# Kernel tuning notes

Measured on AMD Instinct MI355X. Metric: run time of the kernel, lower is better.

## Reference

```python
import jax, jax.numpy as jnp
import numpy as np

DIM = 384
WIN = 7
HEADS = 12
N = WIN * WIN
B_ = 4096
NW = 64


def _relative_position_index(ws: int) -> np.ndarray:
    coords = np.stack(np.meshgrid(np.arange(ws), np.arange(ws), indexing='ij'))  # (2, ws, ws)
    flat = coords.reshape(2, -1)  # (2, N)
    rel = flat[:, :, None] - flat[:, None, :]  # (2, N, N)
    rel = rel.transpose(1, 2, 0).copy()  # (N, N, 2)
    rel[:, :, 0] += ws - 1
    rel[:, :, 1] += ws - 1
    rel[:, :, 0] *= 2 * ws - 1
    return rel.sum(-1).astype(np.int32)  # (N, N)


def setup_inputs() -> dict:
    key = jax.random.key(0)
    ks = jax.random.split(key, 6)
    x = jax.random.normal(ks[0], (B_, N, DIM), dtype=jnp.float32)
    mask = jnp.zeros((NW, N, N), dtype=jnp.float32)
    bias_table = 0.02 * jax.random.normal(ks[1], ((2 * WIN - 1) ** 2, HEADS), dtype=jnp.float32)
    qkv_w = jax.random.normal(ks[2], (3 * DIM, DIM), dtype=jnp.float32) / np.sqrt(DIM)
    qkv_b = jnp.zeros((3 * DIM,), dtype=jnp.float32)
    proj_w = jax.random.normal(ks[3], (DIM, DIM), dtype=jnp.float32) / np.sqrt(DIM)
    proj_b = jnp.zeros((DIM,), dtype=jnp.float32)
    rel_index = jnp.asarray(_relative_position_index(WIN))  # (N, N) int32
    return {"x": x, "mask": mask, "bias_table": bias_table, "qkv_w": qkv_w,
            "qkv_b": qkv_b, "proj_w": proj_w, "proj_b": proj_b, "rel_index": rel_index}


def reference(x, mask, bias_table, qkv_w, qkv_b, proj_w, proj_b, rel_index):
    Bw, n, c = x.shape
    h = bias_table.shape[1]
    d = c // h
    scale = d ** (-0.5)
    # qkv projection: (Bw, n, 3, h, d)
    qkv = (x @ qkv_w.T + qkv_b).reshape(Bw, n, 3, h, d)
    qkv = jnp.transpose(qkv, (2, 0, 3, 1, 4))  # (3, Bw, h, n, d)
    q, k, v = qkv[0], qkv[1], qkv[2]
    attn = jnp.einsum('bhqd,bhkd->bhqk', q * scale, k)  # (Bw, h, n, n)
    bias = bias_table[rel_index]  # (n, n, h)
    attn = attn + jnp.transpose(bias, (2, 0, 1))[None]  # broadcast over Bw
    nW = mask.shape[0]
    attn = attn.reshape(Bw // nW, nW, h, n, n) + mask[None, :, None]
    attn = attn.reshape(Bw, h, n, n)
    attn = jax.nn.softmax(attn, axis=-1)
    out = jnp.einsum('bhqk,bhkd->bhqd', attn, v)  # (Bw, h, n, d)
    out = jnp.transpose(out, (0, 2, 1, 3)).reshape(Bw, n, c)
    return out @ proj_w.T + proj_b
```

## Files before the change

kernel.cpp:

```cpp
#include <hip/hip_runtime.h>
#include <hip/hip_bf16.h>

#define DIM   384
#define NWIN  49
#define HEADS 12
#define SCALE 0.17677669529663687f

typedef unsigned short ushort;
using bf16x8 = __attribute__((ext_vector_type(8))) short;
using u16x4  = __attribute__((ext_vector_type(4))) ushort;
using f32x4  = __attribute__((ext_vector_type(4))) float;

__device__ __forceinline__ ushort f2bf(float f) {
  unsigned u = __float_as_uint(f);
  u += 0x7fff + ((u >> 16) & 1);
  return (ushort)(u >> 16);
}

typedef __attribute__((address_space(1))) const void gas_void;
typedef __attribute__((address_space(3))) void las_void;

__device__ __forceinline__ void gload16(const ushort* g, ushort* l) {
  __builtin_amdgcn_global_load_lds((gas_void*)g, (las_void*)l, 16, 0, 0);
}

__global__ void prep_kernel(const float* __restrict__ qkv_w, const float* __restrict__ proj_w,
                            const float* __restrict__ bias_table, const int* __restrict__ rel_index,
                            const float* __restrict__ mask, const float* __restrict__ qkv_b,
                            ushort* __restrict__ wqb, ushort* __restrict__ wpb,
                            float* __restrict__ qbF, float* __restrict__ bmL) {
  int i0 = blockIdx.x * 256 + threadIdx.x;
  int stride = gridDim.x * 256;
  for (int i = i0; i < 1152 * 384; i += stride) {
    float v = qkv_w[i];
    if (i < 384 * 384) v *= SCALE;
    wqb[i] = f2bf(v);
  }
  for (int i = i0; i < 384 * 384; i += stride) wpb[i] = f2bf(proj_w[i]);
  for (int i = i0; i < 1152; i += stride) qbF[i] = qkv_b[i] * (i < 384 ? SCALE : 1.f);
  for (int i = i0; i < 64 * HEADS * 4 * 4 * 4 * 64; i += stride) {
    int l = i & 63, r = (i >> 6) & 3, kt = (i >> 8) & 3, wq = (i >> 10) & 3;
    int hw = i >> 12;
    int h = hw % 12, wdx = hw / 12;
    int q = wq * 16 + (l >> 4) * 4 + r;
    int key = kt * 16 + (l & 15);
    float v;
    if (q < NWIN)
      v = (key < NWIN) ? bias_table[rel_index[q * NWIN + key] * HEADS + h]
                         + mask[wdx * (NWIN * NWIN) + q * NWIN + key]
                       : -3.0e38f;
    else
      v = 0.f;
    bmL[i] = v;
  }
}

#define WB_OFF 0
#define QS_OFF 24576
#define KS_OFF 29696
#define VT_OFF 34816
#define AO_OFF 39424
#define SMEM_US 77056

__global__ __launch_bounds__(512, 2) void winattn_kernel(
    const float* __restrict__ x, const float* __restrict__ qbF,
    const float* __restrict__ proj_b, const ushort* __restrict__ wqb,
    const ushort* __restrict__ wpb, const float* __restrict__ bmL,
    float* __restrict__ out)
{
  extern __shared__ ushort smem[];
  ushort* wb = smem + WB_OFF;
  ushort* ao = smem + AO_OFF;

  const int blk = blockIdx.x;
  const int tid = threadIdx.x;
  const int w = tid >> 6, l = tid & 63;
  const int c = l & 15, g = l >> 4;
  const int wm = w >> 1, wn = w & 1;
  const int win = w >> 2, wq = w & 3;
  const float LOG2E = 1.4426950408889634f;

  ushort* qsw = smem + QS_OFF + win * 2560;
  ushort* ksw = smem + KS_OFF + win * 2560;
  ushort* vtw = smem + VT_OFF + win * 2304;
  ushort* psw = qsw;

  auto stage_qkv = [&](int h, int kc, int buf) {
    #pragma unroll
    for (int s = 0; s < 3; ++s) {
      int i = s * 512 + tid;
      int n = i >> 4, g16 = i & 15;
      int grow = (n >> 5) * 384 + h * 32 + (n & 31);
      int sg = (g16 & 8) | ((g16 & 7) ^ (n & 7));
      gload16(wqb + (size_t)grow * DIM + kc * 128 + (sg << 3),
              wb + buf * 12288 + i * 8);
    }
  };
  auto stage_proj = [&](int nb, int kc, int buf) {
    #pragma unroll
    for (int s = 0; s < 3; ++s) {
      int i = s * 512 + tid;
      int n = i >> 4, g16 = i & 15;
      int grow = nb * 96 + n;
      int sg = (g16 & 8) | ((g16 & 7) ^ (n & 7));
      gload16(wpb + (size_t)grow * DIM + kc * 128 + (sg << 3),
              wb + buf * 12288 + i * 8);
    }
  };

  bf16x8 areg[2][12] = {};
  auto compute_qkv = [&](int kcC, int buf, f32x4 (&acc)[2][3]) {
    const ushort* wcb = wb + buf * 12288;
    #pragma unroll
    for (int kk = 0; kk < 4; ++kk) {
      int sB = ((kk * 4 + g) ^ (c & 7)) << 3;
      #pragma unroll
      for (int nt = 0; nt < 3; ++nt) {
        int n = (wn * 3 + nt) * 16 + c;
        bf16x8 bb = *(const bf16x8*)&wcb[n * 128 + sB];
        acc[0][nt] = __builtin_amdgcn_mfma_f32_16x16x32_bf16(areg[0][kcC * 4 + kk], bb, acc[0][nt], 0, 0, 0);
        acc[1][nt] = __builtin_amdgcn_mfma_f32_16x16x32_bf16(areg[1][kcC * 4 + kk], bb, acc[1][nt], 0, 0, 0);
      }
    }
  };
  auto compute_proj = [&](int kcC, int buf, f32x4 (&acc)[2][3]) {
    const ushort* wcb = wb + buf * 12288;
    int r0 = wm * 32 + c;      if (r0 >= 98) r0 -= 64;
    int r1 = wm * 32 + 16 + c; if (r1 >= 98) r1 -= 64;
    #pragma unroll
    for (int kk = 0; kk < 4; ++kk) {
      int p = kcC * 16 + kk * 4 + g;
      int sw = (p ^ (c & 7)) << 3;
      bf16x8 a0 = *(const bf16x8*)&ao[r0 * 384 + sw];
      bf16x8 a1 = *(const bf16x8*)&ao[r1 * 384 + sw];
      int sB = ((kk * 4 + g) ^ (c & 7)) << 3;
      #pragma unroll
      for (int nt = 0; nt < 3; ++nt) {
        int n = (wn * 3 + nt) * 16 + c;
        bf16x8 bb = *(const bf16x8*)&wcb[n * 128 + sB];
        acc[0][nt] = __builtin_amdgcn_mfma_f32_16x16x32_bf16(a0, bb, acc[0][nt], 0, 0, 0);
        acc[1][nt] = __builtin_amdgcn_mfma_f32_16x16x32_bf16(a1, bb, acc[1][nt], 0, 0, 0);
      }
    }
  };

  stage_qkv(0, 0, 0);
  stage_qkv(0, 1, 1);
  {
    const float* xb = x + (size_t)blk * (2 * NWIN * DIM);
    for (int i = tid; i < 9408; i += 512) {
      float4 f = ((const float4*)xb)[i];
      int row = i / 96;
      int c4 = i - row * 96;
      int k = c4 * 4;
      int gr = k >> 3;
      u16x4 v4 = { f2bf(f.x), f2bf(f.y), f2bf(f.z), f2bf(f.w) };
      *(u16x4*)&ao[row * 384 + ((gr ^ (row & 7)) << 3) + (k & 7)] = v4;
    }
  }
  __syncthreads();

  #pragma unroll
  for (int mt = 0; mt < 2; ++mt) {
    int row = wm * 32 + mt * 16 + c;
    int wi = row >> 6, tok = row & 63;
    if (tok < NWIN) {
      int ar = wi * 49 + tok;
      #pragma unroll
      for (int kg = 0; kg < 12; ++kg) {
        int gx = kg * 4 + g;
        areg[mt][kg] = *(const bf16x8*)&ao[ar * 384 + ((gx ^ (ar & 7)) << 3)];
      }
    }
  }

  for (int h = 0; h < HEADS; ++h) {
    f32x4 acc[2][3] = {};
    const int par = h & 1;

    compute_qkv(0, par, acc);
    __syncthreads();
    stage_qkv(h, 2, par);

    compute_qkv(1, par ^ 1, acc);
    __syncthreads();
    if (h < 11) stage_qkv(h + 1, 0, par ^ 1); else stage_proj(0, 0, par ^ 1);

    compute_qkv(2, par, acc);
    __syncthreads();
    if (h < 11) stage_qkv(h + 1, 1, par); else stage_proj(0, 1, par);

    {
      int winE = wm >> 1;
      ushort* qsE = smem + QS_OFF + winE * 2560;
      ushort* ksE = smem + KS_OFF + winE * 2560;
      ushort* vtE = smem + VT_OFF + winE * 2304;
      #pragma unroll
      for (int nt = 0; nt < 3; ++nt) {
        int gnt = wn * 3 + nt;
        int which = gnt >> 1;
        int d = (gnt & 1) * 16 + c;
        float qb_ = qbF[which * 384 + h * 32 + d];
        #pragma unroll
        for (int mt = 0; mt < 2; ++mt) {
          #pragma unroll
          for (int r = 0; r < 4; ++r) {
            int tok = (wm & 1) * 32 + mt * 16 + g * 4 + r;
            float v = acc[mt][nt][r] + qb_;
            if (which == 0)      qsE[tok * 40 + d] = f2bf(v);
            else if (which == 1) ksE[tok * 40 + d] = f2bf(v);
            else                 vtE[d * 72 + tok] = f2bf(v);
          }
        }
      }
    }
    __syncthreads();

    const int wdx = ((blk << 1) + win) & 63;
    const float* bw = bmL + ((size_t)((wdx * HEADS + h) * 4 + wq) << 10) + l;
    float bmv[4][4];
    #pragma unroll
    for (int kt = 0; kt < 4; ++kt)
      #pragma unroll
      for (int r = 0; r < 4; ++r)
        bmv[kt][r] = bw[(kt * 4 + r) << 6];

    f32x4 sacc[4] = {};
    {
      bf16x8 aq = *(const bf16x8*)&qsw[(wq * 16 + c) * 40 + g * 8];
      #pragma unroll
      for (int kt = 0; kt < 4; ++kt) {
        bf16x8 bk = *(const bf16x8*)&ksw[(kt * 16 + c) * 40 + g * 8];
        sacc[kt] = __builtin_amdgcn_mfma_f32_16x16x32_bf16(aq, bk, sacc[kt], 0, 0, 0);
      }
    }
    float p[4][4];
    #pragma unroll
    for (int r = 0; r < 4; ++r) {
      float s0 = sacc[0][r] + bmv[0][r], s1 = sacc[1][r] + bmv[1][r];
      float s2 = sacc[2][r] + bmv[2][r], s3 = sacc[3][r] + bmv[3][r];
      float mx = fmaxf(fmaxf(s0, s1), fmaxf(s2, s3));
      mx = fmaxf(mx, __shfl_xor(mx, 1, 64));
      mx = fmaxf(mx, __shfl_xor(mx, 2, 64));
      mx = fmaxf(mx, __shfl_xor(mx, 4, 64));
      mx = fmaxf(mx, __shfl_xor(mx, 8, 64));
      float p0 = __builtin_exp2f((s0 - mx) * LOG2E);
      float p1 = __builtin_exp2f((s1 - mx) * LOG2E);
      float p2 = __builtin_exp2f((s2 - mx) * LOG2E);
      float p3 = __builtin_exp2f((s3 - mx) * LOG2E);
      float sum = p0 + p1 + p2 + p3;
      sum += __shfl_xor(sum, 1, 64);
      sum += __shfl_xor(sum, 2, 64);
      sum += __shfl_xor(sum, 4, 64);
      sum += __shfl_xor(sum, 8, 64);
      float inv = 1.0f / sum;
      p[0][r] = p0 * inv; p[1][r] = p1 * inv; p[2][r] = p2 * inv; p[3][r] = p3 * inv;
    }
    f32x4 pacc2[2] = {};
    #pragma unroll
    for (int kkh = 0; kkh < 2; ++kkh) {
      #pragma unroll
      for (int t = 0; t < 2; ++t) {
        int kt = kkh * 2 + t;
        #pragma unroll
        for (int r = 0; r < 4; ++r)
          psw[(wq * 16 + g * 4 + r) * 40 + t * 16 + c] = f2bf(p[kt][r]);
      }
      bf16x8 ap = *(const bf16x8*)&psw[(wq * 16 + c) * 40 + g * 8];
      #pragma unroll
      for (int dt = 0; dt < 2; ++dt) {
        bf16x8 bv = *(const bf16x8*)&vtw[(dt * 16 + c) * 72 + kkh * 32 + g * 8];
        pacc2[dt] = __builtin_amdgcn_mfma_f32_16x16x32_bf16(ap, bv, pacc2[dt], 0, 0, 0);
      }
    }
    #pragma unroll
    for (int dt = 0; dt < 2; ++dt) {
      int gr0 = h * 4 + dt * 2 + (c >> 3);
      #pragma unroll
      for (int rp = 0; rp < 2; ++rp) {
        int tok0 = wq * 16 + g * 4 + rp * 2;
        int row0 = win * 49 + tok0;
        if (tok0 < NWIN)
          ao[row0 * 384 + (((gr0 ^ (row0 & 7)) << 3) | (c & 7))] = f2bf(pacc2[dt][2 * rp]);
        if (tok0 + 1 < NWIN)
          ao[(row0 + 1) * 384 + (((gr0 ^ ((row0 + 1) & 7)) << 3) | (c & 7))] = f2bf(pacc2[dt][2 * rp + 1]);
      }
    }
  }

  __syncthreads();

  for (int nb = 0; nb < 4; ++nb) {
    f32x4 acc[2][3] = {};
    const int pb0 = (nb * 3) & 1;

    compute_proj(0, pb0, acc);
    __syncthreads();
    stage_proj(nb, 2, pb0);

    compute_proj(1, pb0 ^ 1, acc);
    __syncthreads();
    if (nb < 3) stage_proj(nb + 1, 0, pb0 ^ 1);

    compute_proj(2, pb0, acc);
    __syncthreads();
    if (nb < 3) stage_proj(nb + 1, 1, pb0);

    #pragma unroll
    for (int nt = 0; nt < 3; ++nt) {
      int col = nb * 96 + (wn * 3 + nt) * 16 + c;
      float pb = proj_b[col];
      #pragma unroll
      for (int mt = 0; mt < 2; ++mt) {
        #pragma unroll
        for (int r = 0; r < 4; ++r) {
          int mrow = wm * 32 + mt * 16 + g * 4 + r;
          if (mrow < 98) {
            int wi = mrow >= NWIN;
            int tok = mrow - (wi ? NWIN : 0);
            out[((size_t)((blk << 1) + wi) * NWIN + tok) * DIM + col] =
                acc[mt][nt][r] + pb;
          }
        }
      }
    }
  }
}

extern "C" void kernel_launch(void* const* d_in, const int* in_sizes, int n_in,
                              void* d_out, int out_size, void* d_ws, size_t ws_size,
                              hipStream_t stream) {
  const float* x          = (const float*)d_in[0];
  const float* mask       = (const float*)d_in[1];
  const float* bias_table = (const float*)d_in[2];
  const float* qkv_w      = (const float*)d_in[3];
  const float* qkv_b      = (const float*)d_in[4];
  const float* proj_w     = (const float*)d_in[5];
  const float* proj_b     = (const float*)d_in[6];
  const int*   rel_index  = (const int*)d_in[7];
  float* out = (float*)d_out;

  ushort* wqb = (ushort*)d_ws;
  ushort* wpb = (ushort*)((char*)d_ws + 884736);
  float*  qbF = (float*)((char*)d_ws + 1179648);
  float*  bmL = (float*)((char*)d_ws + 1184256);

  hipFuncSetAttribute((const void*)winattn_kernel,
                      hipFuncAttributeMaxDynamicSharedMemorySize, SMEM_US * 2);

  prep_kernel<<<1024, 256, 0, stream>>>(qkv_w, proj_w, bias_table, rel_index, mask, qkv_b,
                                        wqb, wpb, qbF, bmL);
  winattn_kernel<<<2048, 512, SMEM_US * 2, stream>>>(
      x, qbF, proj_b, wqb, wpb, bmL, out);
}
```

Baseline: 816.6 us.

## Process one window per block and load weights directly into registers

Each block now handles a single window with 256 threads instead of two windows with 512 threads, launching 4096 blocks. The double-buffered LDS staging of weight tiles through global_load_lds is removed. Each wave instead loads its bf16 weight fragments straight from global memory into registers, relying on L2 for reuse. The bias/mask table layout is changed so each lane reads a float4, and the LDS swizzle now uses row&15. This gives up the sharing of staged weights across waves and across two windows, so each block does more redundant global weight traffic in exchange for simpler code, fewer barriers and smaller LDS.

```diff
diff --git a/kernel.cpp b/kernel.cpp
--- a/kernel.cpp
+++ b/kernel.cpp
@@ -17,18 +17,11 @@
   return (ushort)(u >> 16);
 }
 
-typedef __attribute__((address_space(1))) const void gas_void;
-typedef __attribute__((address_space(3))) void las_void;
-
-__device__ __forceinline__ void gload16(const ushort* g, ushort* l) {
-  __builtin_amdgcn_global_load_lds((gas_void*)g, (las_void*)l, 16, 0, 0);
-}
-
 __global__ void prep_kernel(const float* __restrict__ qkv_w, const float* __restrict__ proj_w,
                             const float* __restrict__ bias_table, const int* __restrict__ rel_index,
                             const float* __restrict__ mask, const float* __restrict__ qkv_b,
                             ushort* __restrict__ wqb, ushort* __restrict__ wpb,
-                            float* __restrict__ qbF, float* __restrict__ bmL) {
+                            float* __restrict__ qbF, float* __restrict__ bmF) {
   int i0 = blockIdx.x * 256 + threadIdx.x;
   int stride = gridDim.x * 256;
   for (int i = i0; i < 1152 * 384; i += stride) {
@@ -38,12 +31,12 @@
   }
   for (int i = i0; i < 384 * 384; i += stride) wpb[i] = f2bf(proj_w[i]);
   for (int i = i0; i < 1152; i += stride) qbF[i] = qkv_b[i] * (i < 384 ? SCALE : 1.f);
-  for (int i = i0; i < 64 * HEADS * 4 * 4 * 4 * 64; i += stride) {
-    int l = i & 63, r = (i >> 6) & 3, kt = (i >> 8) & 3, wq = (i >> 10) & 3;
+  for (int i = i0; i < 64 * HEADS * 4 * 4 * 64 * 4; i += stride) {
+    int r = i & 3, lane = (i >> 2) & 63, kt = (i >> 8) & 3, wq = (i >> 10) & 3;
     int hw = i >> 12;
-    int h = hw % 12, wdx = hw / 12;
-    int q = wq * 16 + (l >> 4) * 4 + r;
-    int key = kt * 16 + (l & 15);
+    int h = hw % HEADS, wdx = hw / HEADS;
+    int q = wq * 16 + (lane >> 4) * 4 + r;
+    int key = kt * 16 + (lane & 15);
     float v;
     if (q < NWIN)
       v = (key < NWIN) ? bias_table[rel_index[q * NWIN + key] * HEADS + h]
@@ -51,186 +44,94 @@
                        : -3.0e38f;
     else
       v = 0.f;
-    bmL[i] = v;
-  }
-}
-
-#define WB_OFF 0
-#define QS_OFF 24576
-#define KS_OFF 29696
-#define VT_OFF 34816
-#define AO_OFF 39424
-#define SMEM_US 77056
-
-__global__ __launch_bounds__(512, 2) void winattn_kernel(
+    bmF[i] = v;
+  }
+}
+
+__global__ __launch_bounds__(256, 2) void winattn_kernel(
     const float* __restrict__ x, const float* __restrict__ qbF,
     const float* __restrict__ proj_b, const ushort* __restrict__ wqb,
-    const ushort* __restrict__ wpb, const float* __restrict__ bmL,
+    const ushort* __restrict__ wpb, const float* __restrict__ bmF,
     float* __restrict__ out)
 {
-  extern __shared__ ushort smem[];
-  ushort* wb = smem + WB_OFF;
-  ushort* ao = smem + AO_OFF;
+  __shared__ ushort qs[64 * 40];
+  __shared__ ushort ks[64 * 40];
+  __shared__ ushort vt[32 * 72];
+  __shared__ ushort ao[NWIN * 384];
 
   const int blk = blockIdx.x;
   const int tid = threadIdx.x;
   const int w = tid >> 6, l = tid & 63;
   const int c = l & 15, g = l >> 4;
   const int wm = w >> 1, wn = w & 1;
-  const int win = w >> 2, wq = w & 3;
+  const int wq = w;
+  const int wdx = blk & 63;
   const float LOG2E = 1.4426950408889634f;
 
-  ushort* qsw = smem + QS_OFF + win * 2560;
-  ushort* ksw = smem + KS_OFF + win * 2560;
-  ushort* vtw = smem + VT_OFF + win * 2304;
-  ushort* psw = qsw;
-
-  auto stage_qkv = [&](int h, int kc, int buf) {
-    #pragma unroll
-    for (int s = 0; s < 3; ++s) {
-      int i = s * 512 + tid;
-      int n = i >> 4, g16 = i & 15;
-      int grow = (n >> 5) * 384 + h * 32 + (n & 31);
-      int sg = (g16 & 8) | ((g16 & 7) ^ (n & 7));
-      gload16(wqb + (size_t)grow * DIM + kc * 128 + (sg << 3),
-              wb + buf * 12288 + i * 8);
-    }
-  };
-  auto stage_proj = [&](int nb, int kc, int buf) {
-    #pragma unroll
-    for (int s = 0; s < 3; ++s) {
-      int i = s * 512 + tid;
-      int n = i >> 4, g16 = i & 15;
-      int grow = nb * 96 + n;
-      int sg = (g16 & 8) | ((g16 & 7) ^ (n & 7));
-      gload16(wpb + (size_t)grow * DIM + kc * 128 + (sg << 3),
-              wb + buf * 12288 + i * 8);
-    }
-  };
+  {
+    const float* xb = x + (size_t)blk * (NWIN * DIM);
+    for (int i = tid; i < 4704; i += 256) {
+      float4 f = ((const float4*)xb)[i];
+      int row = i / 96, c4 = i - row * 96;
+      int gr = (c4 >> 1) ^ (row & 15);
+      u16x4 v4 = { f2bf(f.x), f2bf(f.y), f2bf(f.z), f2bf(f.w) };
+      *(u16x4*)&ao[row * 384 + (gr << 3) + (c4 & 1) * 4] = v4;
+    }
+  }
+  __syncthreads();
 
   bf16x8 areg[2][12] = {};
-  auto compute_qkv = [&](int kcC, int buf, f32x4 (&acc)[2][3]) {
-    const ushort* wcb = wb + buf * 12288;
-    #pragma unroll
-    for (int kk = 0; kk < 4; ++kk) {
-      int sB = ((kk * 4 + g) ^ (c & 7)) << 3;
-      #pragma unroll
-      for (int nt = 0; nt < 3; ++nt) {
-        int n = (wn * 3 + nt) * 16 + c;
-        bf16x8 bb = *(const bf16x8*)&wcb[n * 128 + sB];
-        acc[0][nt] = __builtin_amdgcn_mfma_f32_16x16x32_bf16(areg[0][kcC * 4 + kk], bb, acc[0][nt], 0, 0, 0);
-        acc[1][nt] = __builtin_amdgcn_mfma_f32_16x16x32_bf16(areg[1][kcC * 4 + kk], bb, acc[1][nt], 0, 0, 0);
-      }
-    }
-  };
-  auto compute_proj = [&](int kcC, int buf, f32x4 (&acc)[2][3]) {
-    const ushort* wcb = wb + buf * 12288;
-    int r0 = wm * 32 + c;      if (r0 >= 98) r0 -= 64;
-    int r1 = wm * 32 + 16 + c; if (r1 >= 98) r1 -= 64;
-    #pragma unroll
-    for (int kk = 0; kk < 4; ++kk) {
-      int p = kcC * 16 + kk * 4 + g;
-      int sw = (p ^ (c & 7)) << 3;
-      bf16x8 a0 = *(const bf16x8*)&ao[r0 * 384 + sw];
-      bf16x8 a1 = *(const bf16x8*)&ao[r1 * 384 + sw];
-      int sB = ((kk * 4 + g) ^ (c & 7)) << 3;
-      #pragma unroll
-      for (int nt = 0; nt < 3; ++nt) {
-        int n = (wn * 3 + nt) * 16 + c;
-        bf16x8 bb = *(const bf16x8*)&wcb[n * 128 + sB];
-        acc[0][nt] = __builtin_amdgcn_mfma_f32_16x16x32_bf16(a0, bb, acc[0][nt], 0, 0, 0);
-        acc[1][nt] = __builtin_amdgcn_mfma_f32_16x16x32_bf16(a1, bb, acc[1][nt], 0, 0, 0);
-      }
-    }
-  };
-
-  stage_qkv(0, 0, 0);
-  stage_qkv(0, 1, 1);
-  {
-    const float* xb = x + (size_t)blk * (2 * NWIN * DIM);
-    for (int i = tid; i < 9408; i += 512) {
-      float4 f = ((const float4*)xb)[i];
-      int row = i / 96;
-      int c4 = i - row * 96;
-      int k = c4 * 4;
-      int gr = k >> 3;
-      u16x4 v4 = { f2bf(f.x), f2bf(f.y), f2bf(f.z), f2bf(f.w) };
-      *(u16x4*)&ao[row * 384 + ((gr ^ (row & 7)) << 3) + (k & 7)] = v4;
-    }
-  }
-  __syncthreads();
-
   #pragma unroll
   for (int mt = 0; mt < 2; ++mt) {
     int row = wm * 32 + mt * 16 + c;
-    int wi = row >> 6, tok = row & 63;
-    if (tok < NWIN) {
-      int ar = wi * 49 + tok;
+    if (row < NWIN) {
+      #pragma unroll
+      for (int kg = 0; kg < 12; ++kg)
+        areg[mt][kg] = *(const bf16x8*)&ao[row * 384 + (((kg * 4 + g) ^ (row & 15)) << 3)];
+    }
+  }
+
+  for (int h = 0; h < HEADS; ++h) {
+    #pragma unroll
+    for (int m = 0; m < 3; ++m) {
+      const int d = wn * 16 + c;
+      const ushort* bsrc = wqb + ((size_t)(m * 384 + h * 32 + d)) * DIM + g * 8;
+      bf16x8 breg[12];
+      #pragma unroll
+      for (int kg = 0; kg < 12; ++kg)
+        breg[kg] = *(const bf16x8*)(bsrc + kg * 32);
+      f32x4 acc[2] = {};
       #pragma unroll
       for (int kg = 0; kg < 12; ++kg) {
-        int gx = kg * 4 + g;
-        areg[mt][kg] = *(const bf16x8*)&ao[ar * 384 + ((gx ^ (ar & 7)) << 3)];
-      }
-    }
-  }
-
-  for (int h = 0; h < HEADS; ++h) {
-    f32x4 acc[2][3] = {};
-    const int par = h & 1;
-
-    compute_qkv(0, par, acc);
+        acc[0] = __builtin_amdgcn_mfma_f32_16x16x32_bf16(areg[0][kg], breg[kg], acc[0], 0, 0, 0);
+        acc[1] = __builtin_amdgcn_mfma_f32_16x16x32_bf16(areg[1][kg], breg[kg], acc[1], 0, 0, 0);
+      }
+      float qb_ = qbF[m * 384 + h * 32 + d];
+      #pragma unroll
+      for (int mt = 0; mt < 2; ++mt) {
+        #pragma unroll
+        for (int r = 0; r < 4; ++r) {
+          int tok = wm * 32 + mt * 16 + g * 4 + r;
+          float v = acc[mt][r] + qb_;
+          if (m == 0)      qs[tok * 40 + d] = f2bf(v);
+          else if (m == 1) ks[tok * 40 + d] = f2bf(v);
+          else             vt[d * 72 + tok] = f2bf(v);
+        }
+      }
+    }
     __syncthreads();
-    stage_qkv(h, 2, par);
-
-    compute_qkv(1, par ^ 1, acc);
-    __syncthreads();
-    if (h < 11) stage_qkv(h + 1, 0, par ^ 1); else stage_proj(0, 0, par ^ 1);
-
-    compute_qkv(2, par, acc);
-    __syncthreads();
-    if (h < 11) stage_qkv(h + 1, 1, par); else stage_proj(0, 1, par);
-
-    {
-      int winE = wm >> 1;
-      ushort* qsE = smem + QS_OFF + winE * 2560;
-      ushort* ksE = smem + KS_OFF + winE * 2560;
-      ushort* vtE = smem + VT_OFF + winE * 2304;
-      #pragma unroll
-      for (int nt = 0; nt < 3; ++nt) {
-        int gnt = wn * 3 + nt;
-        int which = gnt >> 1;
-        int d = (gnt & 1) * 16 + c;
-        float qb_ = qbF[which * 384 + h * 32 + d];
-        #pragma unroll
-        for (int mt = 0; mt < 2; ++mt) {
-          #pragma unroll
-          for (int r = 0; r < 4; ++r) {
-            int tok = (wm & 1) * 32 + mt * 16 + g * 4 + r;
-            float v = acc[mt][nt][r] + qb_;
-            if (which == 0)      qsE[tok * 40 + d] = f2bf(v);
-            else if (which == 1) ksE[tok * 40 + d] = f2bf(v);
-            else                 vtE[d * 72 + tok] = f2bf(v);
-          }
-        }
-      }
-    }
-    __syncthreads();
-
-    const int wdx = ((blk << 1) + win) & 63;
-    const float* bw = bmL + ((size_t)((wdx * HEADS + h) * 4 + wq) << 10) + l;
-    float bmv[4][4];
-    #pragma unroll
-    for (int kt = 0; kt < 4; ++kt)
-      #pragma unroll
-      for (int r = 0; r < 4; ++r)
-        bmv[kt][r] = bw[(kt * 4 + r) << 6];
+
+    const f32x4* bw4 = (const f32x4*)(bmF + ((((size_t)(wdx * HEADS + h)) * 4 + wq) * 4 * 64 + l) * 4);
+    f32x4 bmv[4];
+    #pragma unroll
+    for (int kt = 0; kt < 4; ++kt) bmv[kt] = bw4[kt * 64];
 
     f32x4 sacc[4] = {};
     {
-      bf16x8 aq = *(const bf16x8*)&qsw[(wq * 16 + c) * 40 + g * 8];
+      bf16x8 aq = *(const bf16x8*)&qs[(wq * 16 + c) * 40 + g * 8];
       #pragma unroll
       for (int kt = 0; kt < 4; ++kt) {
-        bf16x8 bk = *(const bf16x8*)&ksw[(kt * 16 + c) * 40 + g * 8];
+        bf16x8 bk = *(const bf16x8*)&ks[(kt * 16 + c) * 40 + g * 8];
         sacc[kt] = __builtin_amdgcn_mfma_f32_16x16x32_bf16(aq, bk, sacc[kt], 0, 0, 0);
       }
     }
@@ -256,7 +157,7 @@
       float inv = 1.0f / sum;
       p[0][r] = p0 * inv; p[1][r] = p1 * inv; p[2][r] = p2 * inv; p[3][r] = p3 * inv;
     }
-    f32x4 pacc2[2] = {};
+    f32x4 pacc[2] = {};
     #pragma unroll
     for (int kkh = 0; kkh < 2; ++kkh) {
       #pragma unroll
@@ -264,64 +165,57 @@
         int kt = kkh * 2 + t;
         #pragma unroll
         for (int r = 0; r < 4; ++r)
-          psw[(wq * 16 + g * 4 + r) * 40 + t * 16 + c] = f2bf(p[kt][r]);
-      }
-      bf16x8 ap = *(const bf16x8*)&psw[(wq * 16 + c) * 40 + g * 8];
+          qs[(wq * 16 + g * 4 + r) * 40 + t * 16 + c] = f2bf(p[kt][r]);
+      }
+      bf16x8 ap = *(const bf16x8*)&qs[(wq * 16 + c) * 40 + g * 8];
       #pragma unroll
       for (int dt = 0; dt < 2; ++dt) {
-        bf16x8 bv = *(const bf16x8*)&vtw[(dt * 16 + c) * 72 + kkh * 32 + g * 8];
-        pacc2[dt] = __builtin_amdgcn_mfma_f32_16x16x32_bf16(ap, bv, pacc2[dt], 0, 0, 0);
+        bf16x8 bv = *(const bf16x8*)&vt[(dt * 16 + c) * 72 + kkh * 32 + g * 8];
+        pacc[dt] = __builtin_amdgcn_mfma_f32_16x16x32_bf16(ap, bv, pacc[dt], 0, 0, 0);
       }
     }
     #pragma unroll
     for (int dt = 0; dt < 2; ++dt) {
       int gr0 = h * 4 + dt * 2 + (c >> 3);
       #pragma unroll
-      for (int rp = 0; rp < 2; ++rp) {
-        int tok0 = wq * 16 + g * 4 + rp * 2;
-        int row0 = win * 49 + tok0;
-        if (tok0 < NWIN)
-          ao[row0 * 384 + (((gr0 ^ (row0 & 7)) << 3) | (c & 7))] = f2bf(pacc2[dt][2 * rp]);
-        if (tok0 + 1 < NWIN)
-          ao[(row0 + 1) * 384 + (((gr0 ^ ((row0 + 1) & 7)) << 3) | (c & 7))] = f2bf(pacc2[dt][2 * rp + 1]);
-      }
-    }
-  }
-
-  __syncthreads();
-
-  for (int nb = 0; nb < 4; ++nb) {
-    f32x4 acc[2][3] = {};
-    const int pb0 = (nb * 3) & 1;
-
-    compute_proj(0, pb0, acc);
+      for (int rr = 0; rr < 4; ++rr) {
+        int tok = wq * 16 + g * 4 + rr;
+        if (tok < NWIN)
+          ao[tok * 384 + (((gr0 ^ (tok & 15)) << 3) | (c & 7))] = f2bf(pacc[dt][rr]);
+      }
+    }
     __syncthreads();
-    stage_proj(nb, 2, pb0);
-
-    compute_proj(1, pb0 ^ 1, acc);
-    __syncthreads();
-    if (nb < 3) stage_proj(nb + 1, 0, pb0 ^ 1);
-
-    compute_proj(2, pb0, acc);
-    __syncthreads();
-    if (nb < 3) stage_proj(nb + 1, 1, pb0);
-
-    #pragma unroll
-    for (int nt = 0; nt < 3; ++nt) {
-      int col = nb * 96 + (wn * 3 + nt) * 16 + c;
-      float pb = proj_b[col];
-      #pragma unroll
-      for (int mt = 0; mt < 2; ++mt) {
-        #pragma unroll
-        for (int r = 0; r < 4; ++r) {
-          int mrow = wm * 32 + mt * 16 + g * 4 + r;
-          if (mrow < 98) {
-            int wi = mrow >= NWIN;
-            int tok = mrow - (wi ? NWIN : 0);
-            out[((size_t)((blk << 1) + wi) * NWIN + tok) * DIM + col] =
-                acc[mt][nt][r] + pb;
-          }
-        }
+  }
+
+  #pragma unroll
+  for (int mt = 0; mt < 2; ++mt) {
+    int row = wm * 32 + mt * 16 + c;
+    int rc = row < NWIN ? row : 0;
+    #pragma unroll
+    for (int kg = 0; kg < 12; ++kg)
+      areg[mt][kg] = *(const bf16x8*)&ao[rc * 384 + (((kg * 4 + g) ^ (rc & 15)) << 3)];
+  }
+  for (int nb = 0; nb < 12; ++nb) {
+    const int col = nb * 32 + wn * 16 + c;
+    const ushort* bsrc = wpb + (size_t)col * DIM + g * 8;
+    bf16x8 breg[12];
+    #pragma unroll
+    for (int kg = 0; kg < 12; ++kg)
+      breg[kg] = *(const bf16x8*)(bsrc + kg * 32);
+    f32x4 acc[2] = {};
+    #pragma unroll
+    for (int kg = 0; kg < 12; ++kg) {
+      acc[0] = __builtin_amdgcn_mfma_f32_16x16x32_bf16(areg[0][kg], breg[kg], acc[0], 0, 0, 0);
+      acc[1] = __builtin_amdgcn_mfma_f32_16x16x32_bf16(areg[1][kg], breg[kg], acc[1], 0, 0, 0);
+    }
+    float pb = proj_b[col];
+    #pragma unroll
+    for (int mt = 0; mt < 2; ++mt) {
+      #pragma unroll
+      for (int r = 0; r < 4; ++r) {
+        int tok = wm * 32 + mt * 16 + g * 4 + r;
+        if (tok < NWIN)
+          out[((size_t)blk * NWIN + tok) * DIM + col] = acc[mt][r] + pb;
       }
     }
   }
@@ -343,13 +237,9 @@
   ushort* wqb = (ushort*)d_ws;
   ushort* wpb = (ushort*)((char*)d_ws + 884736);
   float*  qbF = (float*)((char*)d_ws + 1179648);
-  float*  bmL = (float*)((char*)d_ws + 1184256);
-
-  hipFuncSetAttribute((const void*)winattn_kernel,
-                      hipFuncAttributeMaxDynamicSharedMemorySize, SMEM_US * 2);
+  float*  bmF = (float*)((char*)d_ws + 1184256);
 
   prep_kernel<<<1024, 256, 0, stream>>>(qkv_w, proj_w, bias_table, rel_index, mask, qkv_b,
-                                        wqb, wpb, qbF, bmL);
-  winattn_kernel<<<2048, 512, SMEM_US * 2, stream>>>(
-      x, qbF, proj_b, wqb, wpb, bmL, out);
-}
+                                        wqb, wpb, qbF, bmF);
+  winattn_kernel<<<4096, 256, 0, stream>>>(x, qbF, proj_b, wqb, wpb, bmF, out);
+}
```

Measured after the change: 1.270 ms. 1.56x slower.

## Split fused window attention into per-window QKV-attention and tiled projection GEMM kernels

Applied to the files above, without the earlier changes.

Replaces the single fused kernel with a qkv_attn kernel that handles one window per 256-thread block and writes bf16 attention output to a global workspace, followed by a separate 128x128-tiled proj GEMM kernel. The bias/mask table layout is transposed so each lane reads contiguous float4 values. The fused kernel is kept as a fallback when the workspace is too small. The split is meant to improve occupancy and give the projection GEMM better tiling, at the cost of a roughly 150MB bf16 round trip through global memory.

```diff
diff --git a/kernel.cpp b/kernel.cpp
--- a/kernel.cpp
+++ b/kernel.cpp
@@ -28,7 +28,7 @@
                             const float* __restrict__ bias_table, const int* __restrict__ rel_index,
                             const float* __restrict__ mask, const float* __restrict__ qkv_b,
                             ushort* __restrict__ wqb, ushort* __restrict__ wpb,
-                            float* __restrict__ qbF, float* __restrict__ bmL) {
+                            float* __restrict__ qbF, float* __restrict__ bmF) {
   int i0 = blockIdx.x * 256 + threadIdx.x;
   int stride = gridDim.x * 256;
   for (int i = i0; i < 1152 * 384; i += stride) {
@@ -38,12 +38,12 @@
   }
   for (int i = i0; i < 384 * 384; i += stride) wpb[i] = f2bf(proj_w[i]);
   for (int i = i0; i < 1152; i += stride) qbF[i] = qkv_b[i] * (i < 384 ? SCALE : 1.f);
-  for (int i = i0; i < 64 * HEADS * 4 * 4 * 4 * 64; i += stride) {
-    int l = i & 63, r = (i >> 6) & 3, kt = (i >> 8) & 3, wq = (i >> 10) & 3;
+  for (int i = i0; i < 64 * HEADS * 4 * 4 * 64 * 4; i += stride) {
+    int r = i & 3, lane = (i >> 2) & 63, kt = (i >> 8) & 3, wq = (i >> 10) & 3;
     int hw = i >> 12;
-    int h = hw % 12, wdx = hw / 12;
-    int q = wq * 16 + (l >> 4) * 4 + r;
-    int key = kt * 16 + (l & 15);
+    int h = hw % HEADS, wdx = hw / HEADS;
+    int q = wq * 16 + (lane >> 4) * 4 + r;
+    int key = kt * 16 + (lane & 15);
     float v;
     if (q < NWIN)
       v = (key < NWIN) ? bias_table[rel_index[q * NWIN + key] * HEADS + h]
@@ -51,44 +51,33 @@
                        : -3.0e38f;
     else
       v = 0.f;
-    bmL[i] = v;
-  }
-}
-
-#define WB_OFF 0
-#define QS_OFF 24576
-#define KS_OFF 29696
-#define VT_OFF 34816
-#define AO_OFF 39424
-#define SMEM_US 77056
-
-__global__ __launch_bounds__(512, 2) void winattn_kernel(
+    bmF[i] = v;
+  }
+}
+
+__global__ __launch_bounds__(256, 2) void qkv_attn_kernel(
     const float* __restrict__ x, const float* __restrict__ qbF,
-    const float* __restrict__ proj_b, const ushort* __restrict__ wqb,
-    const ushort* __restrict__ wpb, const float* __restrict__ bmL,
-    float* __restrict__ out)
+    const ushort* __restrict__ wqb, const float* __restrict__ bmF,
+    ushort* __restrict__ aog)
 {
-  extern __shared__ ushort smem[];
-  ushort* wb = smem + WB_OFF;
-  ushort* ao = smem + AO_OFF;
+  __shared__ ushort wb[2 * 12288];
+  __shared__ ushort qs[64 * 36];
+  __shared__ ushort ks[64 * 36];
+  __shared__ ushort vt[32 * 74];
 
   const int blk = blockIdx.x;
   const int tid = threadIdx.x;
   const int w = tid >> 6, l = tid & 63;
   const int c = l & 15, g = l >> 4;
   const int wm = w >> 1, wn = w & 1;
-  const int win = w >> 2, wq = w & 3;
+  const int wq = w;
+  const int wdx = blk & 63;
   const float LOG2E = 1.4426950408889634f;
 
-  ushort* qsw = smem + QS_OFF + win * 2560;
-  ushort* ksw = smem + KS_OFF + win * 2560;
-  ushort* vtw = smem + VT_OFF + win * 2304;
-  ushort* psw = qsw;
-
   auto stage_qkv = [&](int h, int kc, int buf) {
     #pragma unroll
-    for (int s = 0; s < 3; ++s) {
-      int i = s * 512 + tid;
+    for (int s = 0; s < 6; ++s) {
+      int i = s * 256 + tid;
       int n = i >> 4, g16 = i & 15;
       int grow = (n >> 5) * 384 + h * 32 + (n & 31);
       int sg = (g16 & 8) | ((g16 & 7) ^ (n & 7));
@@ -96,17 +85,6 @@
               wb + buf * 12288 + i * 8);
     }
   };
-  auto stage_proj = [&](int nb, int kc, int buf) {
-    #pragma unroll
-    for (int s = 0; s < 3; ++s) {
-      int i = s * 512 + tid;
-      int n = i >> 4, g16 = i & 15;
-      int grow = nb * 96 + n;
-      int sg = (g16 & 8) | ((g16 & 7) ^ (n & 7));
-      gload16(wpb + (size_t)grow * DIM + kc * 128 + (sg << 3),
-              wb + buf * 12288 + i * 8);
-    }
-  };
 
   bf16x8 areg[2][12] = {};
   auto compute_qkv = [&](int kcC, int buf, f32x4 (&acc)[2][3]) {
@@ -123,56 +101,30 @@
       }
     }
   };
-  auto compute_proj = [&](int kcC, int buf, f32x4 (&acc)[2][3]) {
-    const ushort* wcb = wb + buf * 12288;
-    int r0 = wm * 32 + c;      if (r0 >= 98) r0 -= 64;
-    int r1 = wm * 32 + 16 + c; if (r1 >= 98) r1 -= 64;
-    #pragma unroll
-    for (int kk = 0; kk < 4; ++kk) {
-      int p = kcC * 16 + kk * 4 + g;
-      int sw = (p ^ (c & 7)) << 3;
-      bf16x8 a0 = *(const bf16x8*)&ao[r0 * 384 + sw];
-      bf16x8 a1 = *(const bf16x8*)&ao[r1 * 384 + sw];
-      int sB = ((kk * 4 + g) ^ (c & 7)) << 3;
-      #pragma unroll
-      for (int nt = 0; nt < 3; ++nt) {
-        int n = (wn * 3 + nt) * 16 + c;
-        bf16x8 bb = *(const bf16x8*)&wcb[n * 128 + sB];
-        acc[0][nt] = __builtin_amdgcn_mfma_f32_16x16x32_bf16(a0, bb, acc[0][nt], 0, 0, 0);
-        acc[1][nt] = __builtin_amdgcn_mfma_f32_16x16x32_bf16(a1, bb, acc[1][nt], 0, 0, 0);
-      }
-    }
-  };
-
-  stage_qkv(0, 0, 0);
-  stage_qkv(0, 1, 1);
+
   {
-    const float* xb = x + (size_t)blk * (2 * NWIN * DIM);
-    for (int i = tid; i < 9408; i += 512) {
+    const float* xb = x + (size_t)blk * (NWIN * DIM);
+    for (int i = tid; i < 4704; i += 256) {
       float4 f = ((const float4*)xb)[i];
-      int row = i / 96;
-      int c4 = i - row * 96;
-      int k = c4 * 4;
-      int gr = k >> 3;
+      int row = i / 96, c4 = i - row * 96;
       u16x4 v4 = { f2bf(f.x), f2bf(f.y), f2bf(f.z), f2bf(f.w) };
-      *(u16x4*)&ao[row * 384 + ((gr ^ (row & 7)) << 3) + (k & 7)] = v4;
+      *(u16x4*)&wb[row * 384 + c4 * 4] = v4;
     }
   }
   __syncthreads();
-
   #pragma unroll
   for (int mt = 0; mt < 2; ++mt) {
     int row = wm * 32 + mt * 16 + c;
-    int wi = row >> 6, tok = row & 63;
-    if (tok < NWIN) {
-      int ar = wi * 49 + tok;
-      #pragma unroll
-      for (int kg = 0; kg < 12; ++kg) {
-        int gx = kg * 4 + g;
-        areg[mt][kg] = *(const bf16x8*)&ao[ar * 384 + ((gx ^ (ar & 7)) << 3)];
-      }
-    }
-  }
+    if (row < NWIN) {
+      #pragma unroll
+      for (int kg = 0; kg < 12; ++kg)
+        areg[mt][kg] = *(const bf16x8*)&wb[row * 384 + kg * 32 + g * 8];
+    }
+  }
+  __syncthreads();
+  stage_qkv(0, 0, 0);
+  stage_qkv(0, 1, 1);
+  __syncthreads();
 
   for (int h = 0; h < HEADS; ++h) {
     f32x4 acc[2][3] = {};
@@ -184,53 +136,43 @@
 
     compute_qkv(1, par ^ 1, acc);
     __syncthreads();
-    if (h < 11) stage_qkv(h + 1, 0, par ^ 1); else stage_proj(0, 0, par ^ 1);
+    if (h < 11) stage_qkv(h + 1, 0, par ^ 1);
 
     compute_qkv(2, par, acc);
     __syncthreads();
-    if (h < 11) stage_qkv(h + 1, 1, par); else stage_proj(0, 1, par);
-
-    {
-      int winE = wm >> 1;
-      ushort* qsE = smem + QS_OFF + winE * 2560;
-      ushort* ksE = smem + KS_OFF + winE * 2560;
-      ushort* vtE = smem + VT_OFF + winE * 2304;
-      #pragma unroll
-      for (int nt = 0; nt < 3; ++nt) {
-        int gnt = wn * 3 + nt;
-        int which = gnt >> 1;
-        int d = (gnt & 1) * 16 + c;
-        float qb_ = qbF[which * 384 + h * 32 + d];
+    if (h < 11) stage_qkv(h + 1, 1, par);
+
+    #pragma unroll
+    for (int nt = 0; nt < 3; ++nt) {
+      int gnt = wn * 3 + nt;
+      int which = gnt >> 1;
+      int d = (gnt & 1) * 16 + c;
+      float qb_ = qbF[which * 384 + h * 32 + d];
+      #pragma unroll
+      for (int mt = 0; mt < 2; ++mt) {
         #pragma unroll
-        for (int mt = 0; mt < 2; ++mt) {
-          #pragma unroll
-          for (int r = 0; r < 4; ++r) {
-            int tok = (wm & 1) * 32 + mt * 16 + g * 4 + r;
-            float v = acc[mt][nt][r] + qb_;
-            if (which == 0)      qsE[tok * 40 + d] = f2bf(v);
-            else if (which == 1) ksE[tok * 40 + d] = f2bf(v);
-            else                 vtE[d * 72 + tok] = f2bf(v);
-          }
+        for (int r = 0; r < 4; ++r) {
+          int tok = wm * 32 + mt * 16 + g * 4 + r;
+          float v = acc[mt][nt][r] + qb_;
+          if (which == 0)      qs[tok * 36 + d] = f2bf(v);
+          else if (which == 1) ks[tok * 36 + d] = f2bf(v);
+          else                 vt[d * 74 + tok] = f2bf(v);
         }
       }
     }
     __syncthreads();
 
-    const int wdx = ((blk << 1) + win) & 63;
-    const float* bw = bmL + ((size_t)((wdx * HEADS + h) * 4 + wq) << 10) + l;
-    float bmv[4][4];
-    #pragma unroll
-    for (int kt = 0; kt < 4; ++kt)
-      #pragma unroll
-      for (int r = 0; r < 4; ++r)
-        bmv[kt][r] = bw[(kt * 4 + r) << 6];
+    const f32x4* bw4 = (const f32x4*)(bmF + ((((size_t)(wdx * HEADS + h)) * 4 + wq) * 4 * 64 + l) * 4);
+    f32x4 bmv[4];
+    #pragma unroll
+    for (int kt = 0; kt < 4; ++kt) bmv[kt] = bw4[kt * 64];
 
     f32x4 sacc[4] = {};
     {
-      bf16x8 aq = *(const bf16x8*)&qsw[(wq * 16 + c) * 40 + g * 8];
+      bf16x8 aq = *(const bf16x8*)&qs[(wq * 16 + c) * 36 + g * 8];
       #pragma unroll
       for (int kt = 0; kt < 4; ++kt) {
-        bf16x8 bk = *(const bf16x8*)&ksw[(kt * 16 + c) * 40 + g * 8];
+        bf16x8 bk = *(const bf16x8*)&ks[(kt * 16 + c) * 36 + g * 8];
         sacc[kt] = __builtin_amdgcn_mfma_f32_16x16x32_bf16(aq, bk, sacc[kt], 0, 0, 0);
       }
     }
@@ -256,6 +198,302 @@
       float inv = 1.0f / sum;
       p[0][r] = p0 * inv; p[1][r] = p1 * inv; p[2][r] = p2 * inv; p[3][r] = p3 * inv;
     }
+    f32x4 pacc[2] = {};
+    #pragma unroll
+    for (int kkh = 0; kkh < 2; ++kkh) {
+      #pragma unroll
+      for (int t = 0; t < 2; ++t) {
+        int kt = kkh * 2 + t;
+        #pragma unroll
+        for (int r = 0; r < 4; ++r)
+          qs[(wq * 16 + g * 4 + r) * 36 + t * 16 + c] = f2bf(p[kt][r]);
+      }
+      bf16x8 ap = *(const bf16x8*)&qs[(wq * 16 + c) * 36 + g * 8];
+      #pragma unroll
+      for (int dt = 0; dt < 2; ++dt) {
+        bf16x8 bv = *(const bf16x8*)&vt[(dt * 16 + c) * 74 + kkh * 32 + g * 8];
+        pacc[dt] = __builtin_amdgcn_mfma_f32_16x16x32_bf16(ap, bv, pacc[dt], 0, 0, 0);
+      }
+    }
+    #pragma unroll
+    for (int dt = 0; dt < 2; ++dt) {
+      #pragma unroll
+      for (int rr = 0; rr < 4; ++rr) {
+        int tok = wq * 16 + g * 4 + rr;
+        if (tok < NWIN)
+          aog[((size_t)blk * NWIN + tok) * DIM + h * 32 + dt * 16 + c] = f2bf(pacc[dt][rr]);
+      }
+    }
+    __syncthreads();
+  }
+}
+
+__global__ __launch_bounds__(256, 2) void proj_kernel(
+    const ushort* __restrict__ ao, const ushort* __restrict__ wpb,
+    const float* __restrict__ proj_b, float* __restrict__ out)
+{
+  extern __shared__ ushort sm3[];
+  ushort* lA = sm3;
+  ushort* lB = sm3 + 16384;
+
+  const int blk = blockIdx.x;
+  const int bM = blk / 3, bN = blk - bM * 3;
+  const int m0 = bM * 128, n0 = bN * 128;
+  const int tid = threadIdx.x;
+  const int w = tid >> 6, l = tid & 63;
+  const int c = l & 15, g = l >> 4;
+  const int wm = w >> 1, wn = w & 1;
+
+  auto stageA = [&](int kc, int buf) {
+    #pragma unroll
+    for (int s = 0; s < 4; ++s) {
+      int i = s * 256 + tid;
+      int row = i >> 3, g16 = i & 7;
+      gload16(ao + (size_t)(m0 + row) * DIM + kc * 64 + ((g16 ^ (row & 7)) << 3),
+              lA + buf * 8192 + i * 8);
+    }
+  };
+  auto stageB = [&](int kc, int buf) {
+    #pragma unroll
+    for (int s = 0; s < 4; ++s) {
+      int i = s * 256 + tid;
+      int row = i >> 3, g16 = i & 7;
+      gload16(wpb + (size_t)(n0 + row) * DIM + kc * 64 + ((g16 ^ (row & 7)) << 3),
+              lB + buf * 8192 + i * 8);
+    }
+  };
+
+  f32x4 acc[4][4] = {};
+  stageA(0, 0); stageB(0, 0);
+  stageA(1, 1); stageB(1, 1);
+  __syncthreads();
+
+  for (int kc = 0; kc < 6; ++kc) {
+    const ushort* A = lA + (kc & 1) * 8192;
+    const ushort* B = lB + (kc & 1) * 8192;
+    #pragma unroll
+    for (int kk = 0; kk < 2; ++kk) {
+      int swz = ((kk * 4 + g) ^ (c & 7)) << 3;
+      bf16x8 af[4], bfr[4];
+      #pragma unroll
+      for (int mt = 0; mt < 4; ++mt)
+        af[mt] = *(const bf16x8*)&A[(wm * 64 + mt * 16 + c) * 64 + swz];
+      #pragma unroll
+      for (int nt = 0; nt < 4; ++nt)
+        bfr[nt] = *(const bf16x8*)&B[(wn * 64 + nt * 16 + c) * 64 + swz];
+      #pragma unroll
+      for (int mt = 0; mt < 4; ++mt)
+        #pragma unroll
+        for (int nt = 0; nt < 4; ++nt)
+          acc[mt][nt] = __builtin_amdgcn_mfma_f32_16x16x32_bf16(af[mt], bfr[nt], acc[mt][nt], 0, 0, 0);
+    }
+    __syncthreads();
+    if (kc + 2 < 6) { stageA(kc + 2, kc & 1); stageB(kc + 2, kc & 1); }
+  }
+
+  #pragma unroll
+  for (int nt = 0; nt < 4; ++nt) {
+    int col = n0 + wn * 64 + nt * 16 + c;
+    float pb = proj_b[col];
+    #pragma unroll
+    for (int mt = 0; mt < 4; ++mt) {
+      #pragma unroll
+      for (int r = 0; r < 4; ++r) {
+        int row = m0 + wm * 64 + mt * 16 + g * 4 + r;
+        out[(size_t)row * DIM + col] = acc[mt][nt][r] + pb;
+      }
+    }
+  }
+}
+
+#define WB_OFF 0
+#define QS_OFF 24576
+#define KS_OFF 29696
+#define VT_OFF 34816
+#define AO_OFF 39424
+#define SMEM_US 77056
+
+__global__ __launch_bounds__(512, 2) void winattn_fused(
+    const float* __restrict__ x, const float* __restrict__ qbF,
+    const float* __restrict__ proj_b, const ushort* __restrict__ wqb,
+    const ushort* __restrict__ wpb, const float* __restrict__ bmF,
+    float* __restrict__ out)
+{
+  extern __shared__ ushort smem[];
+  ushort* wb = smem + WB_OFF;
+  ushort* ao = smem + AO_OFF;
+
+  const int blk = blockIdx.x;
+  const int tid = threadIdx.x;
+  const int w = tid >> 6, l = tid & 63;
+  const int c = l & 15, g = l >> 4;
+  const int wm = w >> 1, wn = w & 1;
+  const int win = w >> 2, wq = w & 3;
+  const float LOG2E = 1.4426950408889634f;
+
+  ushort* qsw = smem + QS_OFF + win * 2560;
+  ushort* ksw = smem + KS_OFF + win * 2560;
+  ushort* vtw = smem + VT_OFF + win * 2304;
+  ushort* psw = qsw;
+
+  auto stage_qkv = [&](int h, int kc, int buf) {
+    #pragma unroll
+    for (int s = 0; s < 3; ++s) {
+      int i = s * 512 + tid;
+      int n = i >> 4, g16 = i & 15;
+      int grow = (n >> 5) * 384 + h * 32 + (n & 31);
+      int sg = (g16 & 8) | ((g16 & 7) ^ (n & 7));
+      gload16(wqb + (size_t)grow * DIM + kc * 128 + (sg << 3), wb + buf * 12288 + i * 8);
+    }
+  };
+  auto stage_proj = [&](int nb, int kc, int buf) {
+    #pragma unroll
+    for (int s = 0; s < 3; ++s) {
+      int i = s * 512 + tid;
+      int n = i >> 4, g16 = i & 15;
+      int grow = nb * 96 + n;
+      int sg = (g16 & 8) | ((g16 & 7) ^ (n & 7));
+      gload16(wpb + (size_t)grow * DIM + kc * 128 + (sg << 3), wb + buf * 12288 + i * 8);
+    }
+  };
+
+  bf16x8 areg[2][12] = {};
+  auto compute_qkv = [&](int kcC, int buf, f32x4 (&acc)[2][3]) {
+    const ushort* wcb = wb + buf * 12288;
+    #pragma unroll
+    for (int kk = 0; kk < 4; ++kk) {
+      int sB = ((kk * 4 + g) ^ (c & 7)) << 3;
+      #pragma unroll
+      for (int nt = 0; nt < 3; ++nt) {
+        int n = (wn * 3 + nt) * 16 + c;
+        bf16x8 bb = *(const bf16x8*)&wcb[n * 128 + sB];
+        acc[0][nt] = __builtin_amdgcn_mfma_f32_16x16x32_bf16(areg[0][kcC * 4 + kk], bb, acc[0][nt], 0, 0, 0);
+        acc[1][nt] = __builtin_amdgcn_mfma_f32_16x16x32_bf16(areg[1][kcC * 4 + kk], bb, acc[1][nt], 0, 0, 0);
+      }
+    }
+  };
+  auto compute_proj = [&](int kcC, int buf, f32x4 (&acc)[2][3]) {
+    const ushort* wcb = wb + buf * 12288;
+    int r0 = wm * 32 + c;      if (r0 >= 98) r0 -= 64;
+    int r1 = wm * 32 + 16 + c; if (r1 >= 98) r1 -= 64;
+    #pragma unroll
+    for (int kk = 0; kk < 4; ++kk) {
+      int p = kcC * 16 + kk * 4 + g;
+      int sw = (p ^ (c & 7)) << 3;
+      bf16x8 a0 = *(const bf16x8*)&ao[r0 * 384 + sw];
+      bf16x8 a1 = *(const bf16x8*)&ao[r1 * 384 + sw];
+      int sB = ((kk * 4 + g) ^ (c & 7)) << 3;
+      #pragma unroll
+      for (int nt = 0; nt < 3; ++nt) {
+        int n = (wn * 3 + nt) * 16 + c;
+        bf16x8 bb = *(const bf16x8*)&wcb[n * 128 + sB];
+        acc[0][nt] = __builtin_amdgcn_mfma_f32_16x16x32_bf16(a0, bb, acc[0][nt], 0, 0, 0);
+        acc[1][nt] = __builtin_amdgcn_mfma_f32_16x16x32_bf16(a1, bb, acc[1][nt], 0, 0, 0);
+      }
+    }
+  };
+
+  stage_qkv(0, 0, 0);
+  stage_qkv(0, 1, 1);
+  {
+    const float* xb = x + (size_t)blk * (2 * NWIN * DIM);
+    for (int i = tid; i < 9408; i += 512) {
+      float4 f = ((const float4*)xb)[i];
+      int row = i / 96, c4 = i - row * 96;
+      int k = c4 * 4;
+      int gr = k >> 3;
+      u16x4 v4 = { f2bf(f.x), f2bf(f.y), f2bf(f.z), f2bf(f.w) };
+      *(u16x4*)&ao[row * 384 + ((gr ^ (row & 7)) << 3) + (k & 7)] = v4;
+    }
+  }
+  __syncthreads();
+  #pragma unroll
+  for (int mt = 0; mt < 2; ++mt) {
+    int row = wm * 32 + mt * 16 + c;
+    int wi = row >> 6, tok = row & 63;
+    if (tok < NWIN) {
+      int ar = wi * 49 + tok;
+      #pragma unroll
+      for (int kg = 0; kg < 12; ++kg)
+        areg[mt][kg] = *(const bf16x8*)&ao[ar * 384 + (((kg * 4 + g) ^ (ar & 7)) << 3)];
+    }
+  }
+
+  for (int h = 0; h < HEADS; ++h) {
+    f32x4 acc[2][3] = {};
+    const int par = h & 1;
+    compute_qkv(0, par, acc);
+    __syncthreads();
+    stage_qkv(h, 2, par);
+    compute_qkv(1, par ^ 1, acc);
+    __syncthreads();
+    if (h < 11) stage_qkv(h + 1, 0, par ^ 1); else stage_proj(0, 0, par ^ 1);
+    compute_qkv(2, par, acc);
+    __syncthreads();
+    if (h < 11) stage_qkv(h + 1, 1, par); else stage_proj(0, 1, par);
+    {
+      int winE = wm >> 1;
+      ushort* qsE = smem + QS_OFF + winE * 2560;
+      ushort* ksE = smem + KS_OFF + winE * 2560;
+      ushort* vtE = smem + VT_OFF + winE * 2304;
+      #pragma unroll
+      for (int nt = 0; nt < 3; ++nt) {
+        int gnt = wn * 3 + nt;
+        int which = gnt >> 1;
+        int d = (gnt & 1) * 16 + c;
+        float qb_ = qbF[which * 384 + h * 32 + d];
+        #pragma unroll
+        for (int mt = 0; mt < 2; ++mt) {
+          #pragma unroll
+          for (int r = 0; r < 4; ++r) {
+            int tok = (wm & 1) * 32 + mt * 16 + g * 4 + r;
+            float v = acc[mt][nt][r] + qb_;
+            if (which == 0)      qsE[tok * 40 + d] = f2bf(v);
+            else if (which == 1) ksE[tok * 40 + d] = f2bf(v);
+            else                 vtE[d * 72 + tok] = f2bf(v);
+          }
+        }
+      }
+    }
+    __syncthreads();
+
+    const int wdx = ((blk << 1) + win) & 63;
+    const f32x4* bw4 = (const f32x4*)(bmF + ((((size_t)(wdx * HEADS + h)) * 4 + wq) * 4 * 64 + l) * 4);
+    f32x4 bmv[4];
+    #pragma unroll
+    for (int kt = 0; kt < 4; ++kt) bmv[kt] = bw4[kt * 64];
+
+    f32x4 sacc[4] = {};
+    {
+      bf16x8 aq = *(const bf16x8*)&qsw[(wq * 16 + c) * 40 + g * 8];
+      #pragma unroll
+      for (int kt = 0; kt < 4; ++kt) {
+        bf16x8 bk = *(const bf16x8*)&ksw[(kt * 16 + c) * 40 + g * 8];
+        sacc[kt] = __builtin_amdgcn_mfma_f32_16x16x32_bf16(aq, bk, sacc[kt], 0, 0, 0);
+      }
+    }
+    float p[4][4];
+    #pragma unroll
+    for (int r = 0; r < 4; ++r) {
+      float s0 = sacc[0][r] + bmv[0][r], s1 = sacc[1][r] + bmv[1][r];
+      float s2 = sacc[2][r] + bmv[2][r], s3 = sacc[3][r] + bmv[3][r];
+      float mx = fmaxf(fmaxf(s0, s1), fmaxf(s2, s3));
+      mx = fmaxf(mx, __shfl_xor(mx, 1, 64));
+      mx = fmaxf(mx, __shfl_xor(mx, 2, 64));
+      mx = fmaxf(mx, __shfl_xor(mx, 4, 64));
+      mx = fmaxf(mx, __shfl_xor(mx, 8, 64));
+      float p0 = __builtin_exp2f((s0 - mx) * LOG2E);
+      float p1 = __builtin_exp2f((s1 - mx) * LOG2E);
+      float p2 = __builtin_exp2f((s2 - mx) * LOG2E);
+      float p3 = __builtin_exp2f((s3 - mx) * LOG2E);
+      float sum = p0 + p1 + p2 + p3;
+      sum += __shfl_xor(sum, 1, 64);
+      sum += __shfl_xor(sum, 2, 64);
+      sum += __shfl_xor(sum, 4, 64);
+      sum += __shfl_xor(sum, 8, 64);
+      float inv = 1.0f / sum;
+      p[0][r] = p0 * inv; p[1][r] = p1 * inv; p[2][r] = p2 * inv; p[3][r] = p3 * inv;
+    }
     f32x4 pacc2[2] = {};
     #pragma unroll
     for (int kkh = 0; kkh < 2; ++kkh) {
@@ -277,35 +515,29 @@
     for (int dt = 0; dt < 2; ++dt) {
       int gr0 = h * 4 + dt * 2 + (c >> 3);
       #pragma unroll
-      for (int rp = 0; rp < 2; ++rp) {
-        int tok0 = wq * 16 + g * 4 + rp * 2;
-        int row0 = win * 49 + tok0;
-        if (tok0 < NWIN)
-          ao[row0 * 384 + (((gr0 ^ (row0 & 7)) << 3) | (c & 7))] = f2bf(pacc2[dt][2 * rp]);
-        if (tok0 + 1 < NWIN)
-          ao[(row0 + 1) * 384 + (((gr0 ^ ((row0 + 1) & 7)) << 3) | (c & 7))] = f2bf(pacc2[dt][2 * rp + 1]);
-      }
-    }
+      for (int rr = 0; rr < 4; ++rr) {
+        int tok = wq * 16 + g * 4 + rr;
+        int row0 = win * 49 + tok;
+        if (tok < NWIN)
+          ao[row0 * 384 + (((gr0 ^ (row0 & 7)) << 3) | (c & 7))] = f2bf(pacc2[dt][rr]);
+      }
+    }
+    __syncthreads();
   }
 
   __syncthreads();
-
   for (int nb = 0; nb < 4; ++nb) {
     f32x4 acc[2][3] = {};
     const int pb0 = (nb * 3) & 1;
-
     compute_proj(0, pb0, acc);
     __syncthreads();
     stage_proj(nb, 2, pb0);
-
     compute_proj(1, pb0 ^ 1, acc);
     __syncthreads();
     if (nb < 3) stage_proj(nb + 1, 0, pb0 ^ 1);
-
     compute_proj(2, pb0, acc);
     __syncthreads();
     if (nb < 3) stage_proj(nb + 1, 1, pb0);
-
     #pragma unroll
     for (int nt = 0; nt < 3; ++nt) {
       int col = nb * 96 + (wn * 3 + nt) * 16 + c;
@@ -318,8 +550,7 @@
           if (mrow < 98) {
             int wi = mrow >= NWIN;
             int tok = mrow - (wi ? NWIN : 0);
-            out[((size_t)((blk << 1) + wi) * NWIN + tok) * DIM + col] =
-                acc[mt][nt][r] + pb;
+            out[((size_t)((blk << 1) + wi) * NWIN + tok) * DIM + col] = acc[mt][nt][r] + pb;
           }
         }
       }
@@ -343,13 +574,21 @@
   ushort* wqb = (ushort*)d_ws;
   ushort* wpb = (ushort*)((char*)d_ws + 884736);
   float*  qbF = (float*)((char*)d_ws + 1179648);
-  float*  bmL = (float*)((char*)d_ws + 1184256);
-
-  hipFuncSetAttribute((const void*)winattn_kernel,
-                      hipFuncAttributeMaxDynamicSharedMemorySize, SMEM_US * 2);
+  float*  bmF = (float*)((char*)d_ws + 1184256);
+  ushort* aog = (ushort*)((char*)d_ws + 13767168);
+  const size_t NEED = 13767168ull + 154140672ull;
 
   prep_kernel<<<1024, 256, 0, stream>>>(qkv_w, proj_w, bias_table, rel_index, mask, qkv_b,
-                                        wqb, wpb, qbF, bmL);
-  winattn_kernel<<<2048, 512, SMEM_US * 2, stream>>>(
-      x, qbF, proj_b, wqb, wpb, bmL, out);
-}
+                                        wqb, wpb, qbF, bmF);
+
+  if (ws_size >= NEED) {
+    qkv_attn_kernel<<<4096, 256, 0, stream>>>(x, qbF, wqb, bmF, aog);
+    hipFuncSetAttribute((const void*)proj_kernel,
+                        hipFuncAttributeMaxDynamicSharedMemorySize, 65536);
+    proj_kernel<<<4704, 256, 65536, stream>>>(aog, wpb, proj_b, out);
+  } else {
+    hipFuncSetAttribute((const void*)winattn_fused,
+                        hipFuncAttributeMaxDynamicSharedMemorySize, SMEM_US * 2);
+    winattn_fused<<<2048, 512, SMEM_US * 2, stream>>>(x, qbF, proj_b, wqb, wpb, bmF, out);
+  }
+}
```

New measurement: 798.6 us. 2.2% less time.
